# Kernel optimization log

Hardware: AMD Instinct MI355X
Metric: run time of the kernel (lower is better)

The kernel has to match this reference:

```python
import jax, jax.numpy as jnp
import numpy as np

V, E, H, T = 50000, 256, 512, 5
HD = H // 2          # per-direction LSTM hidden
S = 4096             # sequence length
START, STOP = 3, 4
NEG = -10000.0


def setup_inputs() -> dict:
    key = jax.random.key(0)
    ks = jax.random.split(key, 12)
    nrm = lambda k, shape, sc=0.1: (jax.random.normal(k, shape, jnp.float32) * sc)
    sentence = jax.random.randint(ks[0], (S,), 0, V)
    embed = nrm(ks[1], (V, E), 1.0)
    # torch LSTM gate layout: [i, f, g, o] stacked along first dim (4*HD)
    w_ih_f = nrm(ks[2], (4 * HD, E)); w_hh_f = nrm(ks[3], (4 * HD, HD)); b_f = nrm(ks[4], (4 * HD,))
    w_ih_b = nrm(ks[5], (4 * HD, E)); w_hh_b = nrm(ks[6], (4 * HD, HD)); b_b = nrm(ks[7], (4 * HD,))
    W_tag = nrm(ks[8], (T, H)); b_tag = nrm(ks[9], (T,))
    transitions = jax.random.normal(ks[10], (T, T), jnp.float32)
    transitions = transitions.at[START, :].set(NEG).at[:, STOP].set(NEG)
    return dict(sentence=sentence, embed=embed,
                w_ih_f=w_ih_f, w_hh_f=w_hh_f, b_f=b_f,
                w_ih_b=w_ih_b, w_hh_b=w_hh_b, b_b=b_b,
                W_tag=W_tag, b_tag=b_tag, transitions=transitions)


def _lstm_dir(x, w_ih, w_hh, b, reverse):
    # x: [S, E] -> hidden states [S, HD]; zero initial state (torch default)
    xg = x @ w_ih.T + b  # [S, 4*HD] input projection precomputed
    def step(carry, g_x):
        h, c = carry
        g = g_x + h @ w_hh.T
        i, f, gc, o = jnp.split(g, 4)
        i = jax.nn.sigmoid(i); f = jax.nn.sigmoid(f)
        gc = jnp.tanh(gc); o = jax.nn.sigmoid(o)
        c = f * c + i * gc
        h = o * jnp.tanh(c)
        return (h, c), h
    init = (jnp.zeros((HD,), x.dtype), jnp.zeros((HD,), x.dtype))
    _, hs = jax.lax.scan(step, init, xg, reverse=reverse)
    return hs


def _viterbi(feats, transitions):
    fv0 = jnp.full((T,), NEG, feats.dtype).at[START].set(0.0)
    def vit(fv, feat):
        scores = fv[None, :] + transitions        # [next_tag, prev_tag]
        bp = jnp.argmax(scores, axis=1)
        return jnp.max(scores, axis=1) + feat, bp
    fv, bptrs = jax.lax.scan(vit, fv0, feats)     # bptrs: [S, T]
    terminal = fv + transitions[STOP]
    best = jnp.argmax(terminal)
    score = terminal[best]
    def back(tag, bp):
        return bp[tag], tag
    _, path = jax.lax.scan(back, best, bptrs, reverse=True)  # path: [S]
    return score, path


def reference(sentence, embed, w_ih_f, w_hh_f, b_f, w_ih_b, w_hh_b, b_b, W_tag, b_tag, transitions):
    x = embed[sentence]                                   # [S, E]
    hf = _lstm_dir(x, w_ih_f, w_hh_f, b_f, reverse=False)  # [S, HD]
    hb = _lstm_dir(x, w_ih_b, w_hh_b, b_b, reverse=True)   # [S, HD]
    feats = jnp.concatenate([hf, hb], axis=-1) @ W_tag.T + b_tag  # [S, T]
    score, path = _viterbi(feats, transitions)
    return score, path
```

## Files before the change

### kernel.cpp

```cpp
#include <hip/hip_runtime.h>
#include <math.h>

#define SLEN 4096
#define EDIM 256
#define HDIM 256
#define G4   1024
#define NTAG 5
#define NEGV -10000.0f
#define START_TAG 3
#define STOP_TAG 4

__global__ __launch_bounds__(256) void xg_gemm(
    const float* __restrict__ embed, const int* __restrict__ sent,
    const float* __restrict__ wih_f, const float* __restrict__ b_f,
    const float* __restrict__ wih_b, const float* __restrict__ b_b,
    float* __restrict__ xg_f, float* __restrict__ xg_b) {
  const int dir = blockIdx.z;
  const float* wih  = dir ? wih_b : wih_f;
  const float* bias = dir ? b_b  : b_f;
  float* out        = dir ? xg_b : xg_f;
  const int m0 = blockIdx.x * 64;
  const int n0 = blockIdx.y * 64;

  __shared__ float As[32][64];
  __shared__ float Bs[32][64];
  __shared__ int   srow[64];

  const int tid = threadIdx.x;
  if (tid < 64) srow[tid] = sent[m0 + tid];
  __syncthreads();

  const int tn0 = (tid & 15) * 4;
  const int tm0 = (tid >> 4) * 4;
  float acc[4][4];
#pragma unroll
  for (int i = 0; i < 4; i++)
#pragma unroll
    for (int j = 0; j < 4; j++) acc[i][j] = 0.f;

  const int msl = tid & 63;
  const int k4b = tid >> 6;

  for (int kk = 0; kk < EDIM; kk += 32) {
    __syncthreads();
    {
      const int row = srow[msl];
#pragma unroll
      for (int rep = 0; rep < 2; rep++) {
        const int k4 = k4b + rep * 4;
        const float4 v = *(const float4*)(embed + (size_t)row * EDIM + kk + k4 * 4);
        As[k4 * 4 + 0][msl] = v.x; As[k4 * 4 + 1][msl] = v.y;
        As[k4 * 4 + 2][msl] = v.z; As[k4 * 4 + 3][msl] = v.w;
      }
#pragma unroll
      for (int rep = 0; rep < 2; rep++) {
        const int k4 = k4b + rep * 4;
        const float4 v = *(const float4*)(wih + (size_t)(n0 + msl) * EDIM + kk + k4 * 4);
        Bs[k4 * 4 + 0][msl] = v.x; Bs[k4 * 4 + 1][msl] = v.y;
        Bs[k4 * 4 + 2][msl] = v.z; Bs[k4 * 4 + 3][msl] = v.w;
      }
    }
    __syncthreads();
#pragma unroll
    for (int k = 0; k < 32; k++) {
      const float4 a4 = *(const float4*)&As[k][tm0];
      const float4 b4 = *(const float4*)&Bs[k][tn0];
      const float av[4] = {a4.x, a4.y, a4.z, a4.w};
      const float bv[4] = {b4.x, b4.y, b4.z, b4.w};
#pragma unroll
      for (int i = 0; i < 4; i++)
#pragma unroll
        for (int j = 0; j < 4; j++) acc[i][j] = fmaf(av[i], bv[j], acc[i][j]);
    }
  }

  float bj[4];
#pragma unroll
  for (int j = 0; j < 4; j++) bj[j] = bias[n0 + tn0 + j];
#pragma unroll
  for (int i = 0; i < 4; i++) {
    float4 o4;
    o4.x = acc[i][0] + bj[0]; o4.y = acc[i][1] + bj[1];
    o4.z = acc[i][2] + bj[2]; o4.w = acc[i][3] + bj[3];
    *(float4*)(out + (size_t)(m0 + tm0 + i) * G4 + n0 + tn0) = o4;
  }
}

__global__ __launch_bounds__(512) void lstm_rec(
    const float* __restrict__ whh_f, const float* __restrict__ whh_b,
    const float* __restrict__ xg_f, const float* __restrict__ xg_b,
    float* hf, float* hb, unsigned int* flags ) {
  const int bid = blockIdx.x;
  const int dir = bid >> 3;
  const int w   = bid & 7;
  const float* whh = dir ? whh_b : whh_f;
  const float* xg  = dir ? xg_b  : xg_f;
  float* hout      = dir ? hb    : hf;
  unsigned int* flagbase = flags + dir * 8 * 16;

  const int tid  = threadIdx.x;
  const int r    = tid >> 2;
  const int kq   = tid & 3;
  const int gate = r >> 5;
  const int u    = r & 31;
  const int grow = gate * 256 + w * 32 + u;

  float4 wreg[16];
  {
    const float4* wsrc = (const float4*)(whh + (size_t)grow * HDIM + kq * 64);
#pragma unroll
    for (int i = 0; i < 16; i++) wreg[i] = wsrc[i];
  }

  __shared__ float h_lds[4 * 72];
  __shared__ float xg_lds[128];
  __shared__ float gv_lds[128];

  float c_state = 0.f;
  bool dead = false;

  for (int s = 0; s < SLEN; s++) {
    const int t = dir ? (SLEN - 1 - s) : s;

    float xval = 0.f;
    if (tid < 128) {
      const int gr2 = (tid >> 5) * 256 + w * 32 + (tid & 31);
      xval = xg[(size_t)t * G4 + gr2];
    }

    if (s > 0) {
      if (tid < 8 && !dead) {
        int guard = 0;
        while (__hip_atomic_load(flagbase + tid * 16, __ATOMIC_ACQUIRE,
                                 __HIP_MEMORY_SCOPE_AGENT) < (unsigned)s) {
          if (++guard > (1 << 21)) { dead = true; break; }
        }
      }
    }
    __syncthreads();

    if (tid < 256) {
      float hv = 0.f;
      if (s > 0) {
        const int hidx = dir ? (t + 1) : (t - 1);
        hv = __hip_atomic_load(hout + (size_t)hidx * HDIM + tid,
                               __ATOMIC_RELAXED, __HIP_MEMORY_SCOPE_AGENT);
      }
      h_lds[(tid >> 6) * 72 + (tid & 63)] = hv;
    }
    if (tid < 128) xg_lds[tid] = xval;
    __syncthreads();

    float acc = 0.f;
    const float* hp = &h_lds[kq * 72];
#pragma unroll
    for (int i = 0; i < 16; i++) {
      const float4 h4 = *(const float4*)(hp + i * 4);
      acc = fmaf(wreg[i].x, h4.x, acc);
      acc = fmaf(wreg[i].y, h4.y, acc);
      acc = fmaf(wreg[i].z, h4.z, acc);
      acc = fmaf(wreg[i].w, h4.w, acc);
    }
    acc += __shfl_xor(acc, 1);
    acc += __shfl_xor(acc, 2);
    if (kq == 0) gv_lds[r] = acc + xg_lds[r];
    __syncthreads();

    if (tid < 32) {
      const float iv = gv_lds[tid];
      const float fv = gv_lds[32 + tid];
      const float gv = gv_lds[64 + tid];
      const float ov = gv_lds[96 + tid];
      const float ii = 1.f / (1.f + expf(-iv));
      const float ff = 1.f / (1.f + expf(-fv));
      const float cg = tanhf(gv);
      const float oo = 1.f / (1.f + expf(-ov));
      c_state = ff * c_state + ii * cg;
      const float h = oo * tanhf(c_state);
      __hip_atomic_store(hout + (size_t)t * HDIM + w * 32 + tid, h,
                         __ATOMIC_RELEASE, __HIP_MEMORY_SCOPE_AGENT);
    }
    __syncthreads();

    if (tid == 0) {
      __threadfence();
      __hip_atomic_store(flagbase + w * 16, (unsigned)(s + 1),
                         __ATOMIC_RELEASE, __HIP_MEMORY_SCOPE_AGENT);
    }
  }
}

__global__ __launch_bounds__(256) void feats_k(
    const float* __restrict__ hf, const float* __restrict__ hb,
    const float* __restrict__ Wtag, const float* __restrict__ btag,
    float* __restrict__ feats) {
  const int gw   = (blockIdx.x * 256 + threadIdx.x) >> 6;
  const int lane = threadIdx.x & 63;
  float v[8];
#pragma unroll
  for (int j = 0; j < 4; j++) v[j]     = hf[(size_t)gw * HDIM + lane + 64 * j];
#pragma unroll
  for (int j = 0; j < 4; j++) v[4 + j] = hb[(size_t)gw * HDIM + lane + 64 * j];
#pragma unroll
  for (int n = 0; n < NTAG; n++) {
    float acc = 0.f;
#pragma unroll
    for (int j = 0; j < 8; j++)
      acc = fmaf(v[j], Wtag[n * 512 + lane + 64 * j], acc);
#pragma unroll
    for (int off = 32; off; off >>= 1) acc += __shfl_xor(acc, off);
    if (lane == 0) feats[(size_t)gw * 8 + n] = acc + btag[n];
  }
}

__global__ __launch_bounds__(64) void viterbi_k(
    const float* __restrict__ feats, const float* __restrict__ trans,
    float* __restrict__ outp) {
  __shared__ float fbuf[512 * 8];
  __shared__ unsigned int bp_lds[SLEN];

  const int lane = threadIdx.x;
  const int n = (lane < NTAG) ? lane : 0;
  float trow[NTAG];
#pragma unroll
  for (int p = 0; p < NTAG; p++) trow[p] = trans[n * NTAG + p];
  float fv = (lane == START_TAG) ? 0.f : NEGV;

  for (int chunk = 0; chunk < SLEN; chunk += 512) {
    for (int i = 0; i < 64; i++)
      fbuf[i * 64 + lane] = feats[(size_t)chunk * 8 + i * 64 + lane];
    __syncthreads();
    for (int tt = 0; tt < 512; tt++) {
      float best = __shfl(fv, 0) + trow[0];
      int bestp = 0;
#pragma unroll
      for (int p = 1; p < NTAG; p++) {
        const float sc = __shfl(fv, p) + trow[p];
        if (sc > best) { best = sc; bestp = p; }
      }
      fv = best + fbuf[tt * 8 + n];
      unsigned int word = 0;
#pragma unroll
      for (int p = 0; p < NTAG; p++)
        word |= (unsigned)(__shfl(bestp, p) & 0xF) << (4 * p);
      if (lane == 0) bp_lds[chunk + tt] = word;
    }
    __syncthreads();
  }

  const float term = fv + trans[STOP_TAG * NTAG + n];
  int best = 0;
  float bs = __shfl(term, 0);
#pragma unroll
  for (int p = 1; p < NTAG; p++) {
    const float v = __shfl(term, p);
    if (v > bs) { bs = v; best = p; }
  }
  if (lane == 0) outp[0] = bs;

  __syncthreads();
  int tag = best;
  for (int t = SLEN - 1; t >= 0; t--) {
    if (lane == 0) outp[1 + t] = (float)tag;
    const unsigned int word = bp_lds[t];
    tag = (int)((word >> (4 * tag)) & 0xF);
  }
}

extern "C" void kernel_launch(void* const* d_in, const int* in_sizes, int n_in,
                              void* d_out, int out_size, void* d_ws, size_t ws_size,
                              hipStream_t stream) {
  const int*   sentence = (const int*)d_in[0];
  const float* embed    = (const float*)d_in[1];
  const float* wih_f    = (const float*)d_in[2];
  const float* whh_f    = (const float*)d_in[3];
  const float* b_f      = (const float*)d_in[4];
  const float* wih_b    = (const float*)d_in[5];
  const float* whh_b    = (const float*)d_in[6];
  const float* b_b      = (const float*)d_in[7];
  const float* Wtag     = (const float*)d_in[8];
  const float* btag     = (const float*)d_in[9];
  const float* trans    = (const float*)d_in[10];
  float* out = (float*)d_out;

  float* xg_f  = (float*)d_ws;
  float* xg_b  = xg_f + (size_t)SLEN * G4;
  float* hf    = xg_b + (size_t)SLEN * G4;
  float* hb    = hf   + (size_t)SLEN * HDIM;
  float* feats = hb   + (size_t)SLEN * HDIM;
  unsigned int* flags = (unsigned int*)(feats + (size_t)SLEN * 8);

  hipMemsetAsync(flags, 0, 2 * 8 * 16 * sizeof(unsigned int), stream);

  dim3 gA(SLEN / 64, G4 / 64, 2);
  xg_gemm<<<gA, 256, 0, stream>>>(embed, sentence, wih_f, b_f, wih_b, b_b, xg_f, xg_b);
  lstm_rec<<<16, 512, 0, stream>>>(whh_f, whh_b, xg_f, xg_b, hf, hb, flags);
  feats_k<<<SLEN * 64 / 256, 256, 0, stream>>>(hf, hb, Wtag, btag, feats);
  viterbi_k<<<1, 64, 0, stream>>>(feats, trans, out);
}
```

Before: 11.59 ms.

## Replace flag-based LSTM step sync with sentinel-polled hidden state values

The hidden-state buffers are pre-filled with a sentinel pattern, and each thread spins directly on its own h value until it stops being the sentinel. This removes the separate per-block flag counters, the threadfence, and two of the three per-step barriers. The thread mapping is reordered so all four gates of a unit sit in one wavefront: gate activations are gathered by shuffles instead of an LDS round trip, and the h tile is double-buffered in LDS. The price is relaxed-ordering polling on 256 addresses per step and a memset of the whole h buffer. Correctness also depends on no real h value ever matching the sentinel bit pattern.

```diff
diff --git a/kernel.cpp b/kernel.cpp
--- a/kernel.cpp
+++ b/kernel.cpp
@@ -9,6 +9,7 @@
 #define NEGV -10000.0f
 #define START_TAG 3
 #define STOP_TAG 4
+#define SENT 0x7F7F7F7FU
 
 __global__ __launch_bounds__(256) void xg_gemm(
     const float* __restrict__ embed, const int* __restrict__ sent,
@@ -86,106 +87,99 @@
   }
 }
 
-__global__ __launch_bounds__(512) void lstm_rec(
+__global__ __launch_bounds__(512, 2) void lstm_rec(
     const float* __restrict__ whh_f, const float* __restrict__ whh_b,
     const float* __restrict__ xg_f, const float* __restrict__ xg_b,
-    float* hf, float* hb, unsigned int* flags ) {
+    float* hf, float* hb) {
   const int bid = blockIdx.x;
   const int dir = bid >> 3;
   const int w   = bid & 7;
   const float* whh = dir ? whh_b : whh_f;
   const float* xg  = dir ? xg_b  : xg_f;
   float* hout      = dir ? hb    : hf;
-  unsigned int* flagbase = flags + dir * 8 * 16;
 
   const int tid  = threadIdx.x;
-  const int r    = tid >> 2;
-  const int kq   = tid & 3;
-  const int gate = r >> 5;
-  const int u    = r & 31;
-  const int grow = gate * 256 + w * 32 + u;
+  const int u    = tid >> 4;
+  const int idx  = tid & 15;
+  const int kq   = idx >> 2;
+  const int g    = idx & 3;
+  const int grow = g * 256 + w * 32 + u;
+  const int lane = tid & 63;
+  const int base = lane & ~15;
 
   float4 wreg[16];
   {
     const float4* wsrc = (const float4*)(whh + (size_t)grow * HDIM + kq * 64);
 #pragma unroll
     for (int i = 0; i < 16; i++) wreg[i] = wsrc[i];
-  }
-
-  __shared__ float h_lds[4 * 72];
-  __shared__ float xg_lds[128];
-  __shared__ float gv_lds[128];
+#pragma unroll
+    for (int i = 0; i < 16; i++)
+      asm volatile("" : "+v"(wreg[i].x), "+v"(wreg[i].y),
+                        "+v"(wreg[i].z), "+v"(wreg[i].w));
+  }
+
+  __shared__ __align__(16) float hbuf[2][4][72];
+  __shared__ int sdead;
+  if (tid == 0) sdead = 0;
+  __syncthreads();
 
   float c_state = 0.f;
-  bool dead = false;
 
   for (int s = 0; s < SLEN; s++) {
     const int t = dir ? (SLEN - 1 - s) : s;
 
     float xval = 0.f;
-    if (tid < 128) {
-      const int gr2 = (tid >> 5) * 256 + w * 32 + (tid & 31);
-      xval = xg[(size_t)t * G4 + gr2];
-    }
-
-    if (s > 0) {
-      if (tid < 8 && !dead) {
-        int guard = 0;
-        while (__hip_atomic_load(flagbase + tid * 16, __ATOMIC_ACQUIRE,
-                                 __HIP_MEMORY_SCOPE_AGENT) < (unsigned)s) {
-          if (++guard > (1 << 21)) { dead = true; break; }
-        }
-      }
-    }
-    __syncthreads();
+    if (kq == 0) xval = xg[(size_t)t * G4 + grow];
 
     if (tid < 256) {
       float hv = 0.f;
       if (s > 0) {
-        const int hidx = dir ? (t + 1) : (t - 1);
-        hv = __hip_atomic_load(hout + (size_t)hidx * HDIM + tid,
-                               __ATOMIC_RELAXED, __HIP_MEMORY_SCOPE_AGENT);
-      }
-      h_lds[(tid >> 6) * 72 + (tid & 63)] = hv;
-    }
-    if (tid < 128) xg_lds[tid] = xval;
-    __syncthreads();
-
-    float acc = 0.f;
-    const float* hp = &h_lds[kq * 72];
+        const int tp = dir ? (t + 1) : (t - 1);
+        const unsigned* hp = (const unsigned*)(hout + (size_t)tp * HDIM) + tid;
+        unsigned v = SENT;
+        if (!sdead) {
+          int guard = 0;
+          do {
+            v = __hip_atomic_load(hp, __ATOMIC_RELAXED, __HIP_MEMORY_SCOPE_AGENT);
+            if (v != SENT) break;
+          } while (++guard < (1 << 16));
+        }
+        if (v == SENT) { v = 0u; sdead = 1; }
+        hv = __uint_as_float(v);
+      }
+      hbuf[s & 1][tid >> 6][tid & 63] = hv;
+    }
+    __syncthreads();
+
+    const float* hp = hbuf[s & 1][kq];
+    float a0 = 0.f, a1 = 0.f, a2 = 0.f, a3 = 0.f;
 #pragma unroll
     for (int i = 0; i < 16; i++) {
       const float4 h4 = *(const float4*)(hp + i * 4);
-      acc = fmaf(wreg[i].x, h4.x, acc);
-      acc = fmaf(wreg[i].y, h4.y, acc);
-      acc = fmaf(wreg[i].z, h4.z, acc);
-      acc = fmaf(wreg[i].w, h4.w, acc);
-    }
-    acc += __shfl_xor(acc, 1);
-    acc += __shfl_xor(acc, 2);
-    if (kq == 0) gv_lds[r] = acc + xg_lds[r];
-    __syncthreads();
-
-    if (tid < 32) {
-      const float iv = gv_lds[tid];
-      const float fv = gv_lds[32 + tid];
-      const float gv = gv_lds[64 + tid];
-      const float ov = gv_lds[96 + tid];
-      const float ii = 1.f / (1.f + expf(-iv));
-      const float ff = 1.f / (1.f + expf(-fv));
-      const float cg = tanhf(gv);
-      const float oo = 1.f / (1.f + expf(-ov));
+      a0 = fmaf(wreg[i].x, h4.x, a0);
+      a1 = fmaf(wreg[i].y, h4.y, a1);
+      a2 = fmaf(wreg[i].z, h4.z, a2);
+      a3 = fmaf(wreg[i].w, h4.w, a3);
+    }
+    float acc = (a0 + a1) + (a2 + a3);
+    acc += __shfl_xor(acc, 4);
+    acc += __shfl_xor(acc, 8);
+    if (kq == 0) acc += xval;
+
+    const float fraw = __shfl(acc, base + 1);
+    const float graw = __shfl(acc, base + 2);
+    const float oraw = __shfl(acc, base + 3);
+
+    if (idx == 0) {
+      const float ii = 1.f / (1.f + expf(-acc));
+      const float ff = 1.f / (1.f + expf(-fraw));
+      const float cg = tanhf(graw);
+      const float oo = 1.f / (1.f + expf(-oraw));
       c_state = ff * c_state + ii * cg;
       const float h = oo * tanhf(c_state);
-      __hip_atomic_store(hout + (size_t)t * HDIM + w * 32 + tid, h,
-                         __ATOMIC_RELEASE, __HIP_MEMORY_SCOPE_AGENT);
-    }
-    __syncthreads();
-
-    if (tid == 0) {
-      __threadfence();
-      __hip_atomic_store(flagbase + w * 16, (unsigned)(s + 1),
-                         __ATOMIC_RELEASE, __HIP_MEMORY_SCOPE_AGENT);
+      __hip_atomic_store((unsigned*)(hout + (size_t)t * HDIM + w * 32 + u),
+                         __float_as_uint(h),
+                         __ATOMIC_RELAXED, __HIP_MEMORY_SCOPE_AGENT);
     }
   }
 }
@@ -288,13 +282,12 @@
   float* hf    = xg_b + (size_t)SLEN * G4;
   float* hb    = hf   + (size_t)SLEN * HDIM;
   float* feats = hb   + (size_t)SLEN * HDIM;
-  unsigned int* flags = (unsigned int*)(feats + (size_t)SLEN * 8);
-
-  hipMemsetAsync(flags, 0, 2 * 8 * 16 * sizeof(unsigned int), stream);
+
+  hipMemsetAsync(hf, 0x7F, 2 * (size_t)SLEN * HDIM * sizeof(float), stream);
 
   dim3 gA(SLEN / 64, G4 / 64, 2);
   xg_gemm<<<gA, 256, 0, stream>>>(embed, sentence, wih_f, b_f, wih_b, b_b, xg_f, xg_b);
-  lstm_rec<<<16, 512, 0, stream>>>(whh_f, whh_b, xg_f, xg_b, hf, hb, flags);
+  lstm_rec<<<16, 512, 0, stream>>>(whh_f, whh_b, xg_f, xg_b, hf, hb);
   feats_k<<<SLEN * 64 / 256, 256, 0, stream>>>(hf, hb, Wtag, btag, feats);
   viterbi_k<<<1, 64, 0, stream>>>(feats, trans, out);
 }
```

Result: faster. 10.63 ms (-8.3%).
